# Performance work log

Measured on AMD Instinct MI355X. Metric: run time of the kernel, lower is better.

Reference implementation:

```python
import jax, jax.numpy as jnp
import numpy as np

N_P, N_A = 200_000, 100_000
D_P, D_A, H, OUT = 64, 64, 32, 1
E_PP, E_AP, E_PA = 3_200_000, 1_600_000, 1_600_000


def _lin(key, din, dout, bias=True):
    kw, kb = jax.random.split(key)
    W = jax.random.normal(kw, (din, dout), jnp.float32) * (1.0 / np.sqrt(din))
    if bias:
        b = jax.random.normal(kb, (dout,), jnp.float32) * 0.01
        return W, b
    return W


def setup_inputs() -> dict:
    key = jax.random.key(0)
    ks = jax.random.split(key, 24)
    inp = {}
    inp['x_paper'] = jax.random.normal(ks[0], (N_P, D_P), jnp.float32)
    inp['x_author'] = jax.random.normal(ks[1], (N_A, D_A), jnp.float32)
    inp['src_pp'] = jax.random.randint(ks[2], (E_PP,), 0, N_P)
    inp['dst_pp'] = jax.random.randint(ks[3], (E_PP,), 0, N_P)
    inp['src_ap'] = jax.random.randint(ks[4], (E_AP,), 0, N_A)
    inp['dst_ap'] = jax.random.randint(ks[5], (E_AP,), 0, N_P)
    inp['src_pa'] = jax.random.randint(ks[6], (E_PA,), 0, N_P)
    inp['dst_pa'] = jax.random.randint(ks[7], (E_PA,), 0, N_A)
    # Layer-1 SAGEConv weights per relation: lin_l (neighbor, with bias), lin_r (root, no bias)
    inp['Wl1_pp'], inp['bl1_pp'] = _lin(ks[8], D_P, H)
    inp['Wr1_pp'] = _lin(ks[9], D_P, H, bias=False)
    inp['Wl1_ap'], inp['bl1_ap'] = _lin(ks[10], D_A, H)
    inp['Wr1_ap'] = _lin(ks[11], D_P, H, bias=False)
    inp['Wl1_pa'], inp['bl1_pa'] = _lin(ks[12], D_P, H)
    inp['Wr1_pa'] = _lin(ks[13], D_A, H, bias=False)
    # Layer-2 SAGEConv weights (only relations feeding 'paper' affect the output)
    inp['Wl2_pp'], inp['bl2_pp'] = _lin(ks[14], H, H)
    inp['Wr2_pp'] = _lin(ks[15], H, H, bias=False)
    inp['Wl2_ap'], inp['bl2_ap'] = _lin(ks[16], H, H)
    inp['Wr2_ap'] = _lin(ks[17], H, H, bias=False)
    # Final classifier Linear(32, 1)
    inp['W_lin'], inp['b_lin'] = _lin(ks[18], H, OUT)
    return inp


def _sage_rel(x_src, x_dst, src, dst, Wl, bl, Wr):
    # SAGEConv: lin_l(mean_{j in N(i)} x_j) + lin_r(x_i)
    n_dst = x_dst.shape[0]
    agg = jax.ops.segment_sum(x_src[src], dst, num_segments=n_dst)
    cnt = jax.ops.segment_sum(jnp.ones((src.shape[0],), x_src.dtype), dst, num_segments=n_dst)
    mean = agg / jnp.maximum(cnt, 1.0)[:, None]
    return mean @ Wl + bl + x_dst @ Wr


def reference(x_paper, x_author, src_pp, dst_pp, src_ap, dst_ap, src_pa, dst_pa,
              Wl1_pp, bl1_pp, Wr1_pp, Wl1_ap, bl1_ap, Wr1_ap, Wl1_pa, bl1_pa, Wr1_pa,
              Wl2_pp, bl2_pp, Wr2_pp, Wl2_ap, bl2_ap, Wr2_ap, W_lin, b_lin):
    # Layer 1 (to_hetero: sum per-relation conv outputs per destination type), then relu
    p1 = (_sage_rel(x_paper, x_paper, src_pp, dst_pp, Wl1_pp, bl1_pp, Wr1_pp)
          + _sage_rel(x_author, x_paper, src_ap, dst_ap, Wl1_ap, bl1_ap, Wr1_ap))
    a1 = _sage_rel(x_paper, x_author, src_pa, dst_pa, Wl1_pa, bl1_pa, Wr1_pa)
    p1, a1 = jax.nn.relu(p1), jax.nn.relu(a1)
    # Layer 2: only 'paper' output is consumed downstream
    p2 = (_sage_rel(p1, p1, src_pp, dst_pp, Wl2_pp, bl2_pp, Wr2_pp)
          + _sage_rel(a1, p1, src_ap, dst_ap, Wl2_ap, bl2_ap, Wr2_ap))
    # model_config is None -> plain Linear, no sigmoid/softmax
    return p2 @ W_lin + b_lin
```

## Files before the change

kernel.cpp:

```cpp
#include <hip/hip_runtime.h>


typedef unsigned short ushort_t;
typedef __attribute__((ext_vector_type(8))) short bf16x8;
typedef __attribute__((ext_vector_type(4))) float f32x4;

#define PWBITS 9
#define PWIN   (1 << PWBITS)
#define PCHUNK 4096
#define CAPPAD 2048
#define FW_R   12

__device__ inline ushort_t f2bf(float f) {
    unsigned u = __float_as_uint(f);
    unsigned r = (u + 0x7FFFu + ((u >> 16) & 1u)) >> 16;
    return (ushort_t)r;
}
__device__ inline float bf2f_lo(unsigned u) { return __uint_as_float(u << 16); }
__device__ inline float bf2f_hi(unsigned u) { return __uint_as_float(u & 0xFFFF0000u); }
__device__ inline int ntl(const int* p) { return __builtin_nontemporal_load(p); }

__global__ void prep_weights(
    const float* __restrict__ Wl1_pp, const float* __restrict__ Wr1_pp,
    const float* __restrict__ Wl1_ap, const float* __restrict__ Wr1_ap,
    const float* __restrict__ Wl1_pa, const float* __restrict__ Wr1_pa,
    const float* __restrict__ bl1_pp, const float* __restrict__ bl1_ap,
    const float* __restrict__ bl1_pa,
    const float* __restrict__ Wl2_pp, const float* __restrict__ bl2_pp,
    const float* __restrict__ Wr2_pp,
    const float* __restrict__ Wl2_ap, const float* __restrict__ bl2_ap,
    const float* __restrict__ Wr2_ap,
    const float* __restrict__ W_lin, const float* __restrict__ b_lin,
    float* __restrict__ Wcomb_p,
    float* __restrict__ Wcomb_a,
    ushort_t* __restrict__ Wfrag_p,
    ushort_t* __restrict__ Wfrag_a,
    float* __restrict__ bias_p,
    float* __restrict__ bias_a,
    float* __restrict__ vv)
{
    int t = threadIdx.x;
    for (int idx = t; idx < 64 * 96; idx += 256) {
        int i = idx / 96, j = idx % 96;
        float v;
        if (j < 32)       v = Wl1_pp[i * 32 + j];
        else if (j < 64)  v = Wl1_pa[i * 32 + (j - 32)];
        else              v = Wr1_pp[i * 32 + (j - 64)] + Wr1_ap[i * 32 + (j - 64)];
        Wcomb_p[idx] = v;
    }
    for (int idx = t; idx < 64 * 64; idx += 256) {
        int i = idx / 64, j = idx % 64;
        Wcomb_a[idx] = (j < 32) ? Wl1_ap[i * 32 + j] : Wr1_pa[i * 32 + (j - 32)];
    }
    if (t < 32) {
        bias_p[t] = bl1_pp[t] + bl1_ap[t];
        bias_a[t] = bl1_pa[t];
        float vpp = 0.f, vr = 0.f, vap = 0.f;
        for (int j = 0; j < 32; ++j) {
            float wl = W_lin[j];
            vpp += Wl2_pp[t * 32 + j] * wl;
            vr  += (Wr2_pp[t * 32 + j] + Wr2_ap[t * 32 + j]) * wl;
            vap += Wl2_ap[t * 32 + j] * wl;
        }
        vv[t] = vpp; vv[32 + t] = vr; vv[96 + t] = vap;
    }
    if (t == 0) {
        float c = b_lin[0];
        for (int j = 0; j < 32; ++j) c += (bl2_pp[j] + bl2_ap[j]) * W_lin[j];
        vv[64] = c;
    }
    __syncthreads();
    for (int idx = t; idx < 12 * 64 * 8; idx += 256) {
        int f = idx >> 9, l = (idx >> 3) & 63, j = idx & 7;
        int nt = f >> 1, kh = f & 1;
        int k = kh * 32 + 8 * (l >> 4) + j;
        int n = nt * 16 + (l & 15);
        Wfrag_p[idx] = f2bf(Wcomb_p[k * 96 + n]);
    }
    for (int idx = t; idx < 8 * 64 * 8; idx += 256) {
        int f = idx >> 9, l = (idx >> 3) & 63, j = idx & 7;
        int nt = f >> 1, kh = f & 1;
        int k = kh * 32 + 8 * (l >> 4) + j;
        int n = nt * 16 + (l & 15);
        Wfrag_a[idx] = f2bf(Wcomb_a[k * 64 + n]);
    }
}

__global__ __launch_bounds__(256)
void partition3(
    const int* __restrict__ src0, const int* __restrict__ dst0, int E0,
    unsigned* __restrict__ bk0, int cap0, int nw0, int* __restrict__ wc0,
    const int* __restrict__ src1, const int* __restrict__ dst1, int E1,
    unsigned* __restrict__ bk1, int cap1, int nw1, int* __restrict__ wc1,
    const int* __restrict__ src2, const int* __restrict__ dst2, int E2,
    unsigned* __restrict__ bk2, int cap2, int nw2, int* __restrict__ wc2)
{
    __shared__ int lcnt[PWIN];
    __shared__ int lbase[PWIN];
    int nb0 = (E0 + PCHUNK - 1) / PCHUNK;
    int nb1 = (E1 + PCHUNK - 1) / PCHUNK;
    int b = blockIdx.x;
    const int* src; const int* dst; int E; unsigned* bk; int cap; int nw; int* wc; int chunk;
    if (b < nb0)            { src = src0; dst = dst0; E = E0; bk = bk0; cap = cap0; nw = nw0; wc = wc0; chunk = b; }
    else if (b < nb0 + nb1) { src = src1; dst = dst1; E = E1; bk = bk1; cap = cap1; nw = nw1; wc = wc1; chunk = b - nb0; }
    else                    { src = src2; dst = dst2; E = E2; bk = bk2; cap = cap2; nw = nw2; wc = wc2; chunk = b - nb0 - nb1; }
    int e0 = chunk * PCHUNK;
    int d_[16], s_[16];
#pragma unroll
    for (int r = 0; r < 4; ++r) {
        int base = e0 + r * 1024 + threadIdx.x * 4;
        if (base + 3 < E) {
            int4 dv = *(const int4*)(dst + base);
            int4 sv = *(const int4*)(src + base);
            d_[r * 4 + 0] = dv.x; d_[r * 4 + 1] = dv.y; d_[r * 4 + 2] = dv.z; d_[r * 4 + 3] = dv.w;
            s_[r * 4 + 0] = sv.x; s_[r * 4 + 1] = sv.y; s_[r * 4 + 2] = sv.z; s_[r * 4 + 3] = sv.w;
        } else {
#pragma unroll
            for (int k = 0; k < 4; ++k) {
                int e = base + k;
                d_[r * 4 + k] = (e < E) ? dst[e] : -1;
                s_[r * 4 + k] = 0;
            }
        }
    }
    for (int i = threadIdx.x; i < nw; i += 256) lcnt[i] = 0;
    __syncthreads();
#pragma unroll
    for (int k = 0; k < 16; ++k)
        if (d_[k] >= 0) atomicAdd(&lcnt[((unsigned)d_[k]) >> PWBITS], 1);
    __syncthreads();
    for (int i = threadIdx.x; i < nw; i += 256) {
        int c = lcnt[i];
        lbase[i] = (c > 0) ? atomicAdd(&wc[i * 16], c) : 0;
        lcnt[i] = 0;
    }
    __syncthreads();
#pragma unroll
    for (int k = 0; k < 16; ++k) {
        int d = d_[k];
        if (d >= 0) {
            int w = ((unsigned)d) >> PWBITS;
            int off = lbase[w] + atomicAdd(&lcnt[w], 1);
            if (off < cap)
                bk[(size_t)w * cap + off] =
                    (((unsigned)(d & (PWIN - 1))) << 18) | (unsigned)s_[k];
        }
    }
}

__global__ __launch_bounds__(256)
void fill_win3(
    const unsigned* __restrict__ bk0, const int* __restrict__ wc0, int cap0,
    int* __restrict__ csr0, int* __restrict__ cnt0, int* __restrict__ rs0, int N0, int nw0,
    const unsigned* __restrict__ bk1, const int* __restrict__ wc1, int cap1,
    int* __restrict__ csr1, int* __restrict__ cnt1, int* __restrict__ rs1, int N1, int nw1,
    const unsigned* __restrict__ bk2, const int* __restrict__ wc2, int cap2,
    int* __restrict__ csr2, int* __restrict__ cnt2, int* __restrict__ rs2, int N2, int nw2)
{
    __shared__ int lc[PWIN];
    __shared__ int wsum[4], wpre[4];
    int b = blockIdx.x;
    const unsigned* bk; const int* wc; int cap; int* csr; int* cnt; int* rs; int N; int w;
    if (b < nw0)            { bk = bk0; wc = wc0; cap = cap0; csr = csr0; cnt = cnt0; rs = rs0; N = N0; w = b; }
    else if (b < nw0 + nw1) { bk = bk1; wc = wc1; cap = cap1; csr = csr1; cnt = cnt1; rs = rs1; N = N1; w = b - nw0; }
    else                    { bk = bk2; wc = wc2; cap = cap2; csr = csr2; cnt = cnt2; rs = rs2; N = N2; w = b - nw0 - nw1; }
    int d0 = w << PWBITS;
    int sz = wc[w * 16]; if (sz > cap) sz = cap;
    const unsigned* bkt = bk + (size_t)w * cap;
    uint4 u[FW_R];
#pragma unroll
    for (int r = 0; r < FW_R; ++r) {
        int i4 = r * 1024 + threadIdx.x * 4;
        if (i4 + 3 < sz) {
            u[r] = *(const uint4*)(bkt + i4);
        } else {
            u[r].x = (i4 + 0 < sz) ? bkt[i4 + 0] : 0xFFFFFFFFu;
            u[r].y = (i4 + 1 < sz) ? bkt[i4 + 1] : 0xFFFFFFFFu;
            u[r].z = (i4 + 2 < sz) ? bkt[i4 + 2] : 0xFFFFFFFFu;
            u[r].w = (i4 + 3 < sz) ? bkt[i4 + 3] : 0xFFFFFFFFu;
        }
    }
    for (int i = threadIdx.x; i < PWIN; i += 256) lc[i] = 0;
    __syncthreads();
#pragma unroll
    for (int r = 0; r < FW_R; ++r) {
        if (u[r].x != 0xFFFFFFFFu) atomicAdd(&lc[u[r].x >> 18], 1);
        if (u[r].y != 0xFFFFFFFFu) atomicAdd(&lc[u[r].y >> 18], 1);
        if (u[r].z != 0xFFFFFFFFu) atomicAdd(&lc[u[r].z >> 18], 1);
        if (u[r].w != 0xFFFFFFFFu) atomicAdd(&lc[u[r].w >> 18], 1);
    }
    __syncthreads();
    {
        int i = threadIdx.x * 2;
        int d = d0 + i;
        if (d < N)     cnt[d] = lc[i];
        if (d + 1 < N) cnt[d + 1] = lc[i + 1];
    }
    int t2 = threadIdx.x * 2;
    int v0 = lc[t2], v1 = lc[t2 + 1];
    int ts = v0 + v1;
    int lane = threadIdx.x & 63;
    int wid = threadIdx.x >> 6;
    int incl = ts;
#pragma unroll
    for (int off = 1; off < 64; off <<= 1) {
        int o = __shfl_up(incl, off);
        if (lane >= off) incl += o;
    }
    if (lane == 63) wsum[wid] = incl;
    __syncthreads();
    if (threadIdx.x == 0) {
        int r = 0;
        for (int i = 0; i < 4; ++i) { wpre[i] = r; r += wsum[i]; }
    }
    __syncthreads();
    int run = w * cap + wpre[wid] + (incl - ts);
    lc[t2] = run;
    if (d0 + t2 < N) rs[d0 + t2] = run;
    run += v0;
    lc[t2 + 1] = run;
    if (d0 + t2 + 1 < N) rs[d0 + t2 + 1] = run;
    __syncthreads();
#pragma unroll
    for (int r = 0; r < FW_R; ++r) {
        if (u[r].x != 0xFFFFFFFFu) { int p = atomicAdd(&lc[u[r].x >> 18], 1); csr[p] = (int)(u[r].x & 0x3FFFFu); }
        if (u[r].y != 0xFFFFFFFFu) { int p = atomicAdd(&lc[u[r].y >> 18], 1); csr[p] = (int)(u[r].y & 0x3FFFFu); }
        if (u[r].z != 0xFFFFFFFFu) { int p = atomicAdd(&lc[u[r].z >> 18], 1); csr[p] = (int)(u[r].z & 0x3FFFFu); }
        if (u[r].w != 0xFFFFFFFFu) { int p = atomicAdd(&lc[u[r].w >> 18], 1); csr[p] = (int)(u[r].w & 0x3FFFFu); }
    }
}

__device__ inline bf16x8 cvt8(const float* p) {
    float4 a = *(const float4*)p;
    float4 b = *(const float4*)(p + 4);
    bf16x8 r;
    r[0] = (short)f2bf(a.x); r[1] = (short)f2bf(a.y);
    r[2] = (short)f2bf(a.z); r[3] = (short)f2bf(a.w);
    r[4] = (short)f2bf(b.x); r[5] = (short)f2bf(b.y);
    r[6] = (short)f2bf(b.z); r[7] = (short)f2bf(b.w);
    return r;
}

__global__ __launch_bounds__(256)
void proj_paper_mfma(const float* __restrict__ x, const ushort_t* __restrict__ Wfrag,
                     const float* __restrict__ bias,
                     ushort_t* __restrict__ h_pp, ushort_t* __restrict__ h_pa,
                     float* __restrict__ root_p, int N)
{
    int wave = threadIdx.x >> 6, lane = threadIdx.x & 63;
    int mbase = blockIdx.x * 64 + wave * 16;
    int row = lane & 15, grp = lane >> 4;
    int nA = mbase + row; if (nA > N - 1) nA = N - 1;
    const float* xr = x + (size_t)nA * 64 + grp * 8;
    bf16x8 a0 = cvt8(xr);
    bf16x8 a1 = cvt8(xr + 32);
    f32x4 acc0 = {0.f, 0.f, 0.f, 0.f}, acc1 = acc0, acc2 = acc0, acc3 = acc0;
    float bp0 = bias[row];
    float bp1 = bias[16 + row];
    f32x4 acc4 = {bp0, bp0, bp0, bp0};
    f32x4 acc5 = {bp1, bp1, bp1, bp1};
    const bf16x8* wf = (const bf16x8*)(Wfrag) + lane;
    acc0 = __builtin_amdgcn_mfma_f32_16x16x32_bf16(a0, wf[0 * 64], acc0, 0, 0, 0);
    acc0 = __builtin_amdgcn_mfma_f32_16x16x32_bf16(a1, wf[1 * 64], acc0, 0, 0, 0);
    acc1 = __builtin_amdgcn_mfma_f32_16x16x32_bf16(a0, wf[2 * 64], acc1, 0, 0, 0);
    acc1 = __builtin_amdgcn_mfma_f32_16x16x32_bf16(a1, wf[3 * 64], acc1, 0, 0, 0);
    acc2 = __builtin_amdgcn_mfma_f32_16x16x32_bf16(a0, wf[4 * 64], acc2, 0, 0, 0);
    acc2 = __builtin_amdgcn_mfma_f32_16x16x32_bf16(a1, wf[5 * 64], acc2, 0, 0, 0);
    acc3 = __builtin_amdgcn_mfma_f32_16x16x32_bf16(a0, wf[6 * 64], acc3, 0, 0, 0);
    acc3 = __builtin_amdgcn_mfma_f32_16x16x32_bf16(a1, wf[7 * 64], acc3, 0, 0, 0);
    acc4 = __builtin_amdgcn_mfma_f32_16x16x32_bf16(a0, wf[8 * 64], acc4, 0, 0, 0);
    acc4 = __builtin_amdgcn_mfma_f32_16x16x32_bf16(a1, wf[9 * 64], acc4, 0, 0, 0);
    acc5 = __builtin_amdgcn_mfma_f32_16x16x32_bf16(a0, wf[10 * 64], acc5, 0, 0, 0);
    acc5 = __builtin_amdgcn_mfma_f32_16x16x32_bf16(a1, wf[11 * 64], acc5, 0, 0, 0);
    int col = row;
    int node0 = mbase + grp * 4;
#pragma unroll
    for (int reg = 0; reg < 4; ++reg) {
        int nd = node0 + reg;
        if (nd < N) {
            size_t b32 = (size_t)nd * 32;
            h_pp[b32 + col]        = f2bf(acc0[reg]);
            h_pp[b32 + 16 + col]   = f2bf(acc1[reg]);
            h_pa[b32 + col]        = f2bf(acc2[reg]);
            h_pa[b32 + 16 + col]   = f2bf(acc3[reg]);
            root_p[b32 + col]      = acc4[reg];
            root_p[b32 + 16 + col] = acc5[reg];
        }
    }
}

__global__ __launch_bounds__(256)
void proj_author_mfma(const float* __restrict__ x, const ushort_t* __restrict__ Wfrag,
                      const float* __restrict__ bias,
                      ushort_t* __restrict__ h_ap, float* __restrict__ root_a, int N)
{
    int wave = threadIdx.x >> 6, lane = threadIdx.x & 63;
    int mbase = blockIdx.x * 64 + wave * 16;
    int row = lane & 15, grp = lane >> 4;
    int nA = mbase + row; if (nA > N - 1) nA = N - 1;
    const float* xr = x + (size_t)nA * 64 + grp * 8;
    bf16x8 a0 = cvt8(xr);
    bf16x8 a1 = cvt8(xr + 32);
    f32x4 acc0 = {0.f, 0.f, 0.f, 0.f}, acc1 = acc0;
    float bp0 = bias[row];
    float bp1 = bias[16 + row];
    f32x4 acc2 = {bp0, bp0, bp0, bp0};
    f32x4 acc3 = {bp1, bp1, bp1, bp1};
    const bf16x8* wf = (const bf16x8*)(Wfrag) + lane;
    acc0 = __builtin_amdgcn_mfma_f32_16x16x32_bf16(a0, wf[0 * 64], acc0, 0, 0, 0);
    acc0 = __builtin_amdgcn_mfma_f32_16x16x32_bf16(a1, wf[1 * 64], acc0, 0, 0, 0);
    acc1 = __builtin_amdgcn_mfma_f32_16x16x32_bf16(a0, wf[2 * 64], acc1, 0, 0, 0);
    acc1 = __builtin_amdgcn_mfma_f32_16x16x32_bf16(a1, wf[3 * 64], acc1, 0, 0, 0);
    acc2 = __builtin_amdgcn_mfma_f32_16x16x32_bf16(a0, wf[4 * 64], acc2, 0, 0, 0);
    acc2 = __builtin_amdgcn_mfma_f32_16x16x32_bf16(a1, wf[5 * 64], acc2, 0, 0, 0);
    acc3 = __builtin_amdgcn_mfma_f32_16x16x32_bf16(a0, wf[6 * 64], acc3, 0, 0, 0);
    acc3 = __builtin_amdgcn_mfma_f32_16x16x32_bf16(a1, wf[7 * 64], acc3, 0, 0, 0);
    int col = row;
    int node0 = mbase + grp * 4;
#pragma unroll
    for (int reg = 0; reg < 4; ++reg) {
        int nd = node0 + reg;
        if (nd < N) {
            size_t b32 = (size_t)nd * 32;
            h_ap[b32 + col]        = f2bf(acc0[reg]);
            h_ap[b32 + 16 + col]   = f2bf(acc1[reg]);
            root_a[b32 + col]      = acc2[reg];
            root_a[b32 + 16 + col] = acc3[reg];
        }
    }
}

#define ACC8(A, U) \
    A[0] += bf2f_lo((U).x); A[1] += bf2f_hi((U).x); \
    A[2] += bf2f_lo((U).y); A[3] += bf2f_hi((U).y); \
    A[4] += bf2f_lo((U).z); A[5] += bf2f_hi((U).z); \
    A[6] += bf2f_lo((U).w); A[7] += bf2f_hi((U).w);

__global__ __launch_bounds__(256, 8)
void pull_paper(const ushort_t* __restrict__ h_pp, const ushort_t* __restrict__ h_ap,
                const float* __restrict__ root,
                const int* __restrict__ csr_pp, const int* __restrict__ rs_pp,
                const int* __restrict__ cnt_pp,
                const int* __restrict__ csr_ap, const int* __restrict__ rs_ap,
                const int* __restrict__ cnt_ap,
                const float* __restrict__ vv,
                float* __restrict__ s_pp, float* __restrict__ out, int N)
{
    __shared__ float v0[32], v1[32];
    __shared__ float c2s;
    if (threadIdx.x < 32) { v0[threadIdx.x] = vv[threadIdx.x]; v1[threadIdx.x] = vv[32 + threadIdx.x]; }
    if (threadIdx.x == 0) c2s = vv[64];
    __syncthreads();
    int n = blockIdx.x * 64 + (threadIdx.x >> 2);
    if (n >= N) return;
    int c = threadIdx.x & 3;
    float a[8];
#pragma unroll
    for (int k = 0; k < 8; ++k) a[k] = 0.f;
    int s1 = rs_pp[n], k1 = cnt_pp[n], e1 = s1 + k1;
    int j = s1;
    for (; j + 4 <= e1; j += 4) {
        int i0 = ntl(csr_pp + j), i1 = ntl(csr_pp + j + 1);
        int i2 = ntl(csr_pp + j + 2), i3 = ntl(csr_pp + j + 3);
        uint4 u0 = ((const uint4*)(h_pp + (size_t)i0 * 32))[c];
        uint4 u1 = ((const uint4*)(h_pp + (size_t)i1 * 32))[c];
        uint4 u2 = ((const uint4*)(h_pp + (size_t)i2 * 32))[c];
        uint4 u3 = ((const uint4*)(h_pp + (size_t)i3 * 32))[c];
        ACC8(a, u0) ACC8(a, u1) ACC8(a, u2) ACC8(a, u3)
    }
    for (; j < e1; ++j) {
        uint4 u0 = ((const uint4*)(h_pp + (size_t)ntl(csr_pp + j) * 32))[c];
        ACC8(a, u0)
    }
    float b[8];
#pragma unroll
    for (int k = 0; k < 8; ++k) b[k] = 0.f;
    int s2 = rs_ap[n], k2 = cnt_ap[n], e2 = s2 + k2;
    j = s2;
    for (; j + 4 <= e2; j += 4) {
        int i0 = ntl(csr_ap + j), i1 = ntl(csr_ap + j + 1);
        int i2 = ntl(csr_ap + j + 2), i3 = ntl(csr_ap + j + 3);
        uint4 u0 = ((const uint4*)(h_ap + (size_t)i0 * 32))[c];
        uint4 u1 = ((const uint4*)(h_ap + (size_t)i1 * 32))[c];
        uint4 u2 = ((const uint4*)(h_ap + (size_t)i2 * 32))[c];
        uint4 u3 = ((const uint4*)(h_ap + (size_t)i3 * 32))[c];
        ACC8(b, u0) ACC8(b, u1) ACC8(b, u2) ACC8(b, u3)
    }
    for (; j < e2; ++j) {
        uint4 u0 = ((const uint4*)(h_ap + (size_t)ntl(csr_ap + j) * 32))[c];
        ACC8(b, u0)
    }
    float ipp = 1.0f / fmaxf((float)k1, 1.0f);
    float iap = 1.0f / fmaxf((float)k2, 1.0f);
    const float* rt = root + (size_t)n * 32 + 8 * c;
    float d0 = 0.f, d1 = 0.f;
#pragma unroll
    for (int k = 0; k < 8; ++k) {
        float p = fmaxf(rt[k] + a[k] * ipp + b[k] * iap, 0.f);
        d0 += p * v0[8 * c + k];
        d1 += p * v1[8 * c + k];
    }
    d0 += __shfl_xor(d0, 1); d0 += __shfl_xor(d0, 2);
    d1 += __shfl_xor(d1, 1); d1 += __shfl_xor(d1, 2);
    if (c == 0) { s_pp[n] = d0; out[n] = d1 + c2s; }
}

__global__ __launch_bounds__(256, 8)
void pull_author(const ushort_t* __restrict__ h_pa, const float* __restrict__ root,
                 const int* __restrict__ csr_pa, const int* __restrict__ rs_pa,
                 const int* __restrict__ cnt_pa,
                 const float* __restrict__ vv, float* __restrict__ s_ap, int N)
{
    __shared__ float v0[32];
    if (threadIdx.x < 32) v0[threadIdx.x] = vv[96 + threadIdx.x];
    __syncthreads();
    int n = blockIdx.x * 64 + (threadIdx.x >> 2);
    if (n >= N) return;
    int c = threadIdx.x & 3;
    float a[8];
#pragma unroll
    for (int k = 0; k < 8; ++k) a[k] = 0.f;
    int s1 = rs_pa[n], k1 = cnt_pa[n], e1 = s1 + k1;
    int j = s1;
    for (; j + 4 <= e1; j += 4) {
        int i0 = ntl(csr_pa + j), i1 = ntl(csr_pa + j + 1);
        int i2 = ntl(csr_pa + j + 2), i3 = ntl(csr_pa + j + 3);
        uint4 u0 = ((const uint4*)(h_pa + (size_t)i0 * 32))[c];
        uint4 u1 = ((const uint4*)(h_pa + (size_t)i1 * 32))[c];
        uint4 u2 = ((const uint4*)(h_pa + (size_t)i2 * 32))[c];
        uint4 u3 = ((const uint4*)(h_pa + (size_t)i3 * 32))[c];
        ACC8(a, u0) ACC8(a, u1) ACC8(a, u2) ACC8(a, u3)
    }
    for (; j < e1; ++j) {
        uint4 u0 = ((const uint4*)(h_pa + (size_t)ntl(csr_pa + j) * 32))[c];
        ACC8(a, u0)
    }
    float ip = 1.0f / fmaxf((float)k1, 1.0f);
    const float* rt = root + (size_t)n * 32 + 8 * c;
    float d0 = 0.f;
#pragma unroll
    for (int k = 0; k < 8; ++k) {
        float p = fmaxf(rt[k] + a[k] * ip, 0.f);
        d0 += p * v0[8 * c + k];
    }
    d0 += __shfl_xor(d0, 1); d0 += __shfl_xor(d0, 2);
    if (c == 0) s_ap[n] = d0;
}

__global__ __launch_bounds__(256, 8)
void pull2(const float* __restrict__ s_pp, const float* __restrict__ s_ap,
           const int* __restrict__ csr_pp, const int* __restrict__ rs_pp,
           const int* __restrict__ cnt_pp,
           const int* __restrict__ csr_ap, const int* __restrict__ rs_ap,
           const int* __restrict__ cnt_ap,
           float* __restrict__ out, int N)
{
    int g = (blockIdx.x * blockDim.x + threadIdx.x) >> 2;
    int c = threadIdx.x & 3;
    if (g >= N) return;
    int s1 = rs_pp[g], k1 = cnt_pp[g], e1 = s1 + k1;
    float t = 0.f;
    for (int j = s1 + c; j < e1; j += 4) t += s_pp[ntl(csr_pp + j)];
    int s2 = rs_ap[g], k2 = cnt_ap[g], e2 = s2 + k2;
    float u = 0.f;
    for (int j = s2 + c; j < e2; j += 4) u += s_ap[ntl(csr_ap + j)];
    t += __shfl_xor(t, 1); t += __shfl_xor(t, 2);
    u += __shfl_xor(u, 1); u += __shfl_xor(u, 2);
    if (c == 0) {
        out[g] += t / fmaxf((float)k1, 1.f) + u / fmaxf((float)k2, 1.f);
    }
}

extern "C" void kernel_launch(void* const* d_in, const int* in_sizes, int n_in,
                              void* d_out, int out_size, void* d_ws, size_t ws_size,
                              hipStream_t stream)
{
    const float* x_paper  = (const float*)d_in[0];
    const float* x_author = (const float*)d_in[1];
    const int* src_pp = (const int*)d_in[2];
    const int* dst_pp = (const int*)d_in[3];
    const int* src_ap = (const int*)d_in[4];
    const int* dst_ap = (const int*)d_in[5];
    const int* src_pa = (const int*)d_in[6];
    const int* dst_pa = (const int*)d_in[7];
    const float* Wl1_pp = (const float*)d_in[8];
    const float* bl1_pp = (const float*)d_in[9];
    const float* Wr1_pp = (const float*)d_in[10];
    const float* Wl1_ap = (const float*)d_in[11];
    const float* bl1_ap = (const float*)d_in[12];
    const float* Wr1_ap = (const float*)d_in[13];
    const float* Wl1_pa = (const float*)d_in[14];
    const float* bl1_pa = (const float*)d_in[15];
    const float* Wr1_pa = (const float*)d_in[16];
    const float* Wl2_pp = (const float*)d_in[17];
    const float* bl2_pp = (const float*)d_in[18];
    const float* Wr2_pp = (const float*)d_in[19];
    const float* Wl2_ap = (const float*)d_in[20];
    const float* bl2_ap = (const float*)d_in[21];
    const float* Wr2_ap = (const float*)d_in[22];
    const float* W_lin  = (const float*)d_in[23];
    const float* b_lin  = (const float*)d_in[24];

    const int NP = in_sizes[0] / 64;
    const int NA = in_sizes[1] / 64;
    const int E_PP = in_sizes[2];
    const int E_AP = in_sizes[4];
    const int E_PA = in_sizes[6];

    const int nw_pp = (NP + PWIN - 1) >> PWBITS;
    const int nw_ap = nw_pp;
    const int nw_pa = (NA + PWIN - 1) >> PWBITS;
    const int cap_pp = ((E_PP / nw_pp + CAPPAD) + 3) & ~3;
    const int cap_ap = ((E_AP / nw_ap + CAPPAD) + 3) & ~3;
    const int cap_pa = ((E_PA / nw_pa + CAPPAD) + 3) & ~3;

    char* wp = (char*)d_ws;
    int* wcur = (int*)wp;             wp += (size_t)3 * PWIN * 16 * 4;
    unsigned* bk_pp = (unsigned*)wp;  wp += (size_t)nw_pp * cap_pp * 4;
    unsigned* bk_ap = (unsigned*)wp;  wp += (size_t)nw_ap * cap_ap * 4;
    unsigned* bk_pa = (unsigned*)wp;  wp += (size_t)nw_pa * cap_pa * 4;
    int* csr_pp = (int*)wp;           wp += (size_t)nw_pp * cap_pp * 4;
    int* csr_ap = (int*)wp;           wp += (size_t)nw_ap * cap_ap * 4;
    int* csr_pa = (int*)wp;           wp += (size_t)nw_pa * cap_pa * 4;
    int* cnt    = (int*)wp;           wp += (size_t)(2 * NP + NA) * 4;
    int* rs     = (int*)wp;           wp += (size_t)(2 * NP + NA) * 4;
    ushort_t* h_pp = (ushort_t*)wp;   wp += (size_t)NP * 32 * 2;
    ushort_t* h_pa = (ushort_t*)wp;   wp += (size_t)NP * 32 * 2;
    ushort_t* h_ap = (ushort_t*)wp;   wp += (size_t)NA * 32 * 2;
    float* root_a = (float*)wp;       wp += (size_t)NA * 32 * 4;
    float* s_pp   = (float*)wp;       wp += (size_t)NP * 4;
    float* s_ap   = (float*)wp;       wp += (size_t)NA * 4;
    float* Wcomb_p = (float*)wp;      wp += 64 * 96 * 4;
    float* Wcomb_a = (float*)wp;      wp += 64 * 64 * 4;
    ushort_t* Wfrag_p = (ushort_t*)wp; wp += 12 * 64 * 8 * 2;
    ushort_t* Wfrag_a = (ushort_t*)wp; wp += 8 * 64 * 8 * 2;
    float* bias_p = (float*)wp;       wp += 32 * 4;
    float* bias_a = (float*)wp;       wp += 32 * 4;
    float* vv     = (float*)wp;       wp += 128 * 4;
    float* root_p = (float*)bk_pp;

    int* cnt_pp = cnt,  * cnt_ap = cnt + NP,  * cnt_pa = cnt + 2 * NP;
    int* rs_pp  = rs,   * rs_ap  = rs + NP,   * rs_pa  = rs + 2 * NP;

    float* out = (float*)d_out;

    hipMemsetAsync(wcur, 0, (size_t)3 * PWIN * 16 * 4, stream);

    prep_weights<<<1, 256, 0, stream>>>(
        Wl1_pp, Wr1_pp, Wl1_ap, Wr1_ap, Wl1_pa, Wr1_pa,
        bl1_pp, bl1_ap, bl1_pa,
        Wl2_pp, bl2_pp, Wr2_pp, Wl2_ap, bl2_ap, Wr2_ap,
        W_lin, b_lin, Wcomb_p, Wcomb_a, Wfrag_p, Wfrag_a, bias_p, bias_a, vv);

    int nb_total = (E_PP + PCHUNK - 1) / PCHUNK + (E_AP + PCHUNK - 1) / PCHUNK
                 + (E_PA + PCHUNK - 1) / PCHUNK;
    partition3<<<nb_total, 256, 0, stream>>>(
        src_pp, dst_pp, E_PP, bk_pp, cap_pp, nw_pp, wcur + 0,
        src_ap, dst_ap, E_AP, bk_ap, cap_ap, nw_ap, wcur + PWIN * 16,
        src_pa, dst_pa, E_PA, bk_pa, cap_pa, nw_pa, wcur + 2 * PWIN * 16);

    fill_win3<<<nw_pp + nw_ap + nw_pa, 256, 0, stream>>>(
        bk_pp, wcur + 0,            cap_pp, csr_pp, cnt_pp, rs_pp, NP, nw_pp,
        bk_ap, wcur + PWIN * 16,    cap_ap, csr_ap, cnt_ap, rs_ap, NP, nw_ap,
        bk_pa, wcur + 2 * PWIN * 16, cap_pa, csr_pa, cnt_pa, rs_pa, NA, nw_pa);

    proj_paper_mfma<<<(NP + 63) / 64, 256, 0, stream>>>(
        x_paper, Wfrag_p, bias_p, h_pp, h_pa, root_p, NP);
    proj_author_mfma<<<(NA + 63) / 64, 256, 0, stream>>>(
        x_author, Wfrag_a, bias_a, h_ap, root_a, NA);

    pull_paper<<<(NP + 63) / 64, 256, 0, stream>>>(
        h_pp, h_ap, root_p, csr_pp, rs_pp, cnt_pp, csr_ap, rs_ap, cnt_ap,
        vv, s_pp, out, NP);
    pull_author<<<(NA + 63) / 64, 256, 0, stream>>>(
        h_pa, root_a, csr_pa, rs_pa, cnt_pa, vv, s_ap, NA);

    pull2<<<((size_t)NP * 4 + 255) / 256, 256, 0, stream>>>(
        s_pp, s_ap, csr_pp, rs_pp, cnt_pp, csr_ap, rs_ap, cnt_ap, out, NP);
}
```

Before: 375.6 us.

## Merge paper/author projection and pull kernels into single launches with interleaved gathers

```diff
diff --git a/kernel.cpp b/kernel.cpp
--- a/kernel.cpp
+++ b/kernel.cpp
@@ -242,90 +242,85 @@
 }
 
 __global__ __launch_bounds__(256)
-void proj_paper_mfma(const float* __restrict__ x, const ushort_t* __restrict__ Wfrag,
-                     const float* __restrict__ bias,
-                     ushort_t* __restrict__ h_pp, ushort_t* __restrict__ h_pa,
-                     float* __restrict__ root_p, int N)
+void proj_all(const float* __restrict__ xp, const float* __restrict__ xa,
+              const ushort_t* __restrict__ Wfp, const ushort_t* __restrict__ Wfa,
+              const float* __restrict__ bias_p, const float* __restrict__ bias_a,
+              ushort_t* __restrict__ h_pp, ushort_t* __restrict__ h_pa,
+              ushort_t* __restrict__ h_ap,
+              float* __restrict__ root_p, float* __restrict__ root_a,
+              int NP, int NA, int pbp)
 {
     int wave = threadIdx.x >> 6, lane = threadIdx.x & 63;
-    int mbase = blockIdx.x * 64 + wave * 16;
     int row = lane & 15, grp = lane >> 4;
-    int nA = mbase + row; if (nA > N - 1) nA = N - 1;
-    const float* xr = x + (size_t)nA * 64 + grp * 8;
-    bf16x8 a0 = cvt8(xr);
-    bf16x8 a1 = cvt8(xr + 32);
-    f32x4 acc0 = {0.f, 0.f, 0.f, 0.f}, acc1 = acc0, acc2 = acc0, acc3 = acc0;
-    float bp0 = bias[row];
-    float bp1 = bias[16 + row];
-    f32x4 acc4 = {bp0, bp0, bp0, bp0};
-    f32x4 acc5 = {bp1, bp1, bp1, bp1};
-    const bf16x8* wf = (const bf16x8*)(Wfrag) + lane;
-    acc0 = __builtin_amdgcn_mfma_f32_16x16x32_bf16(a0, wf[0 * 64], acc0, 0, 0, 0);
-    acc0 = __builtin_amdgcn_mfma_f32_16x16x32_bf16(a1, wf[1 * 64], acc0, 0, 0, 0);
-    acc1 = __builtin_amdgcn_mfma_f32_16x16x32_bf16(a0, wf[2 * 64], acc1, 0, 0, 0);
-    acc1 = __builtin_amdgcn_mfma_f32_16x16x32_bf16(a1, wf[3 * 64], acc1, 0, 0, 0);
-    acc2 = __builtin_amdgcn_mfma_f32_16x16x32_bf16(a0, wf[4 * 64], acc2, 0, 0, 0);
-    acc2 = __builtin_amdgcn_mfma_f32_16x16x32_bf16(a1, wf[5 * 64], acc2, 0, 0, 0);
-    acc3 = __builtin_amdgcn_mfma_f32_16x16x32_bf16(a0, wf[6 * 64], acc3, 0, 0, 0);
-    acc3 = __builtin_amdgcn_mfma_f32_16x16x32_bf16(a1, wf[7 * 64], acc3, 0, 0, 0);
-    acc4 = __builtin_amdgcn_mfma_f32_16x16x32_bf16(a0, wf[8 * 64], acc4, 0, 0, 0);
-    acc4 = __builtin_amdgcn_mfma_f32_16x16x32_bf16(a1, wf[9 * 64], acc4, 0, 0, 0);
-    acc5 = __builtin_amdgcn_mfma_f32_16x16x32_bf16(a0, wf[10 * 64], acc5, 0, 0, 0);
-    acc5 = __builtin_amdgcn_mfma_f32_16x16x32_bf16(a1, wf[11 * 64], acc5, 0, 0, 0);
-    int col = row;
-    int node0 = mbase + grp * 4;
-#pragma unroll
-    for (int reg = 0; reg < 4; ++reg) {
-        int nd = node0 + reg;
-        if (nd < N) {
-            size_t b32 = (size_t)nd * 32;
-            h_pp[b32 + col]        = f2bf(acc0[reg]);
-            h_pp[b32 + 16 + col]   = f2bf(acc1[reg]);
-            h_pa[b32 + col]        = f2bf(acc2[reg]);
-            h_pa[b32 + 16 + col]   = f2bf(acc3[reg]);
-            root_p[b32 + col]      = acc4[reg];
-            root_p[b32 + 16 + col] = acc5[reg];
-        }
-    }
-}
-
-__global__ __launch_bounds__(256)
-void proj_author_mfma(const float* __restrict__ x, const ushort_t* __restrict__ Wfrag,
-                      const float* __restrict__ bias,
-                      ushort_t* __restrict__ h_ap, float* __restrict__ root_a, int N)
-{
-    int wave = threadIdx.x >> 6, lane = threadIdx.x & 63;
-    int mbase = blockIdx.x * 64 + wave * 16;
-    int row = lane & 15, grp = lane >> 4;
-    int nA = mbase + row; if (nA > N - 1) nA = N - 1;
-    const float* xr = x + (size_t)nA * 64 + grp * 8;
-    bf16x8 a0 = cvt8(xr);
-    bf16x8 a1 = cvt8(xr + 32);
-    f32x4 acc0 = {0.f, 0.f, 0.f, 0.f}, acc1 = acc0;
-    float bp0 = bias[row];
-    float bp1 = bias[16 + row];
-    f32x4 acc2 = {bp0, bp0, bp0, bp0};
-    f32x4 acc3 = {bp1, bp1, bp1, bp1};
-    const bf16x8* wf = (const bf16x8*)(Wfrag) + lane;
-    acc0 = __builtin_amdgcn_mfma_f32_16x16x32_bf16(a0, wf[0 * 64], acc0, 0, 0, 0);
-    acc0 = __builtin_amdgcn_mfma_f32_16x16x32_bf16(a1, wf[1 * 64], acc0, 0, 0, 0);
-    acc1 = __builtin_amdgcn_mfma_f32_16x16x32_bf16(a0, wf[2 * 64], acc1, 0, 0, 0);
-    acc1 = __builtin_amdgcn_mfma_f32_16x16x32_bf16(a1, wf[3 * 64], acc1, 0, 0, 0);
-    acc2 = __builtin_amdgcn_mfma_f32_16x16x32_bf16(a0, wf[4 * 64], acc2, 0, 0, 0);
-    acc2 = __builtin_amdgcn_mfma_f32_16x16x32_bf16(a1, wf[5 * 64], acc2, 0, 0, 0);
-    acc3 = __builtin_amdgcn_mfma_f32_16x16x32_bf16(a0, wf[6 * 64], acc3, 0, 0, 0);
-    acc3 = __builtin_amdgcn_mfma_f32_16x16x32_bf16(a1, wf[7 * 64], acc3, 0, 0, 0);
-    int col = row;
-    int node0 = mbase + grp * 4;
-#pragma unroll
-    for (int reg = 0; reg < 4; ++reg) {
-        int nd = node0 + reg;
-        if (nd < N) {
-            size_t b32 = (size_t)nd * 32;
-            h_ap[b32 + col]        = f2bf(acc0[reg]);
-            h_ap[b32 + 16 + col]   = f2bf(acc1[reg]);
-            root_a[b32 + col]      = acc2[reg];
-            root_a[b32 + 16 + col] = acc3[reg];
+    if (blockIdx.x < pbp) {
+        int mbase = blockIdx.x * 64 + wave * 16;
+        int nA = mbase + row; if (nA > NP - 1) nA = NP - 1;
+        const float* xr = xp + (size_t)nA * 64 + grp * 8;
+        bf16x8 a0 = cvt8(xr);
+        bf16x8 a1 = cvt8(xr + 32);
+        f32x4 acc0 = {0.f, 0.f, 0.f, 0.f}, acc1 = acc0, acc2 = acc0, acc3 = acc0;
+        float bp0 = bias_p[row];
+        float bp1 = bias_p[16 + row];
+        f32x4 acc4 = {bp0, bp0, bp0, bp0};
+        f32x4 acc5 = {bp1, bp1, bp1, bp1};
+        const bf16x8* wf = (const bf16x8*)(Wfp) + lane;
+        acc0 = __builtin_amdgcn_mfma_f32_16x16x32_bf16(a0, wf[0 * 64], acc0, 0, 0, 0);
+        acc0 = __builtin_amdgcn_mfma_f32_16x16x32_bf16(a1, wf[1 * 64], acc0, 0, 0, 0);
+        acc1 = __builtin_amdgcn_mfma_f32_16x16x32_bf16(a0, wf[2 * 64], acc1, 0, 0, 0);
+        acc1 = __builtin_amdgcn_mfma_f32_16x16x32_bf16(a1, wf[3 * 64], acc1, 0, 0, 0);
+        acc2 = __builtin_amdgcn_mfma_f32_16x16x32_bf16(a0, wf[4 * 64], acc2, 0, 0, 0);
+        acc2 = __builtin_amdgcn_mfma_f32_16x16x32_bf16(a1, wf[5 * 64], acc2, 0, 0, 0);
+        acc3 = __builtin_amdgcn_mfma_f32_16x16x32_bf16(a0, wf[6 * 64], acc3, 0, 0, 0);
+        acc3 = __builtin_amdgcn_mfma_f32_16x16x32_bf16(a1, wf[7 * 64], acc3, 0, 0, 0);
+        acc4 = __builtin_amdgcn_mfma_f32_16x16x32_bf16(a0, wf[8 * 64], acc4, 0, 0, 0);
+        acc4 = __builtin_amdgcn_mfma_f32_16x16x32_bf16(a1, wf[9 * 64], acc4, 0, 0, 0);
+        acc5 = __builtin_amdgcn_mfma_f32_16x16x32_bf16(a0, wf[10 * 64], acc5, 0, 0, 0);
+        acc5 = __builtin_amdgcn_mfma_f32_16x16x32_bf16(a1, wf[11 * 64], acc5, 0, 0, 0);
+        int node0 = mbase + grp * 4;
+#pragma unroll
+        for (int reg = 0; reg < 4; ++reg) {
+            int nd = node0 + reg;
+            if (nd < NP) {
+                size_t b32 = (size_t)nd * 32;
+                h_pp[b32 + row]        = f2bf(acc0[reg]);
+                h_pp[b32 + 16 + row]   = f2bf(acc1[reg]);
+                h_pa[b32 + row]        = f2bf(acc2[reg]);
+                h_pa[b32 + 16 + row]   = f2bf(acc3[reg]);
+                root_p[b32 + row]      = acc4[reg];
+                root_p[b32 + 16 + row] = acc5[reg];
+            }
+        }
+    } else {
+        int mbase = (blockIdx.x - pbp) * 64 + wave * 16;
+        int nA = mbase + row; if (nA > NA - 1) nA = NA - 1;
+        const float* xr = xa + (size_t)nA * 64 + grp * 8;
+        bf16x8 a0 = cvt8(xr);
+        bf16x8 a1 = cvt8(xr + 32);
+        f32x4 acc0 = {0.f, 0.f, 0.f, 0.f}, acc1 = acc0;
+        float bp0 = bias_a[row];
+        float bp1 = bias_a[16 + row];
+        f32x4 acc2 = {bp0, bp0, bp0, bp0};
+        f32x4 acc3 = {bp1, bp1, bp1, bp1};
+        const bf16x8* wf = (const bf16x8*)(Wfa) + lane;
+        acc0 = __builtin_amdgcn_mfma_f32_16x16x32_bf16(a0, wf[0 * 64], acc0, 0, 0, 0);
+        acc0 = __builtin_amdgcn_mfma_f32_16x16x32_bf16(a1, wf[1 * 64], acc0, 0, 0, 0);
+        acc1 = __builtin_amdgcn_mfma_f32_16x16x32_bf16(a0, wf[2 * 64], acc1, 0, 0, 0);
+        acc1 = __builtin_amdgcn_mfma_f32_16x16x32_bf16(a1, wf[3 * 64], acc1, 0, 0, 0);
+        acc2 = __builtin_amdgcn_mfma_f32_16x16x32_bf16(a0, wf[4 * 64], acc2, 0, 0, 0);
+        acc2 = __builtin_amdgcn_mfma_f32_16x16x32_bf16(a1, wf[5 * 64], acc2, 0, 0, 0);
+        acc3 = __builtin_amdgcn_mfma_f32_16x16x32_bf16(a0, wf[6 * 64], acc3, 0, 0, 0);
+        acc3 = __builtin_amdgcn_mfma_f32_16x16x32_bf16(a1, wf[7 * 64], acc3, 0, 0, 0);
+        int node0 = mbase + grp * 4;
+#pragma unroll
+        for (int reg = 0; reg < 4; ++reg) {
+            int nd = node0 + reg;
+            if (nd < NA) {
+                size_t b32 = (size_t)nd * 32;
+                h_ap[b32 + row]        = f2bf(acc0[reg]);
+                h_ap[b32 + 16 + row]   = f2bf(acc1[reg]);
+                root_a[b32 + row]      = acc2[reg];
+                root_a[b32 + 16 + row] = acc3[reg];
+            }
         }
     }
 }
@@ -336,115 +331,125 @@
     A[4] += bf2f_lo((U).z); A[5] += bf2f_hi((U).z); \
     A[6] += bf2f_lo((U).w); A[7] += bf2f_hi((U).w);
 
-__global__ __launch_bounds__(256, 8)
-void pull_paper(const ushort_t* __restrict__ h_pp, const ushort_t* __restrict__ h_ap,
-                const float* __restrict__ root,
-                const int* __restrict__ csr_pp, const int* __restrict__ rs_pp,
-                const int* __restrict__ cnt_pp,
-                const int* __restrict__ csr_ap, const int* __restrict__ rs_ap,
-                const int* __restrict__ cnt_ap,
-                const float* __restrict__ vv,
-                float* __restrict__ s_pp, float* __restrict__ out, int N)
+__global__ __launch_bounds__(256, 6)
+void pull_all(const ushort_t* __restrict__ h_pp, const ushort_t* __restrict__ h_ap,
+              const ushort_t* __restrict__ h_pa,
+              const float* __restrict__ root_p, const float* __restrict__ root_a,
+              const int* __restrict__ csr_pp, const int* __restrict__ rs_pp,
+              const int* __restrict__ cnt_pp,
+              const int* __restrict__ csr_ap, const int* __restrict__ rs_ap,
+              const int* __restrict__ cnt_ap,
+              const int* __restrict__ csr_pa, const int* __restrict__ rs_pa,
+              const int* __restrict__ cnt_pa,
+              const float* __restrict__ vv,
+              float* __restrict__ s_pp, float* __restrict__ s_ap,
+              float* __restrict__ out, int NP, int NA, int pbp)
 {
     __shared__ float v0[32], v1[32];
     __shared__ float c2s;
-    if (threadIdx.x < 32) { v0[threadIdx.x] = vv[threadIdx.x]; v1[threadIdx.x] = vv[32 + threadIdx.x]; }
-    if (threadIdx.x == 0) c2s = vv[64];
-    __syncthreads();
-    int n = blockIdx.x * 64 + (threadIdx.x >> 2);
-    if (n >= N) return;
     int c = threadIdx.x & 3;
-    float a[8];
-#pragma unroll
-    for (int k = 0; k < 8; ++k) a[k] = 0.f;
-    int s1 = rs_pp[n], k1 = cnt_pp[n], e1 = s1 + k1;
-    int j = s1;
-    for (; j + 4 <= e1; j += 4) {
-        int i0 = ntl(csr_pp + j), i1 = ntl(csr_pp + j + 1);
-        int i2 = ntl(csr_pp + j + 2), i3 = ntl(csr_pp + j + 3);
-        uint4 u0 = ((const uint4*)(h_pp + (size_t)i0 * 32))[c];
-        uint4 u1 = ((const uint4*)(h_pp + (size_t)i1 * 32))[c];
-        uint4 u2 = ((const uint4*)(h_pp + (size_t)i2 * 32))[c];
-        uint4 u3 = ((const uint4*)(h_pp + (size_t)i3 * 32))[c];
-        ACC8(a, u0) ACC8(a, u1) ACC8(a, u2) ACC8(a, u3)
-    }
-    for (; j < e1; ++j) {
-        uint4 u0 = ((const uint4*)(h_pp + (size_t)ntl(csr_pp + j) * 32))[c];
-        ACC8(a, u0)
-    }
-    float b[8];
-#pragma unroll
-    for (int k = 0; k < 8; ++k) b[k] = 0.f;
-    int s2 = rs_ap[n], k2 = cnt_ap[n], e2 = s2 + k2;
-    j = s2;
-    for (; j + 4 <= e2; j += 4) {
-        int i0 = ntl(csr_ap + j), i1 = ntl(csr_ap + j + 1);
-        int i2 = ntl(csr_ap + j + 2), i3 = ntl(csr_ap + j + 3);
-        uint4 u0 = ((const uint4*)(h_ap + (size_t)i0 * 32))[c];
-        uint4 u1 = ((const uint4*)(h_ap + (size_t)i1 * 32))[c];
-        uint4 u2 = ((const uint4*)(h_ap + (size_t)i2 * 32))[c];
-        uint4 u3 = ((const uint4*)(h_ap + (size_t)i3 * 32))[c];
-        ACC8(b, u0) ACC8(b, u1) ACC8(b, u2) ACC8(b, u3)
-    }
-    for (; j < e2; ++j) {
-        uint4 u0 = ((const uint4*)(h_ap + (size_t)ntl(csr_ap + j) * 32))[c];
-        ACC8(b, u0)
-    }
-    float ipp = 1.0f / fmaxf((float)k1, 1.0f);
-    float iap = 1.0f / fmaxf((float)k2, 1.0f);
-    const float* rt = root + (size_t)n * 32 + 8 * c;
-    float d0 = 0.f, d1 = 0.f;
-#pragma unroll
-    for (int k = 0; k < 8; ++k) {
-        float p = fmaxf(rt[k] + a[k] * ipp + b[k] * iap, 0.f);
-        d0 += p * v0[8 * c + k];
-        d1 += p * v1[8 * c + k];
-    }
-    d0 += __shfl_xor(d0, 1); d0 += __shfl_xor(d0, 2);
-    d1 += __shfl_xor(d1, 1); d1 += __shfl_xor(d1, 2);
-    if (c == 0) { s_pp[n] = d0; out[n] = d1 + c2s; }
-}
-
-__global__ __launch_bounds__(256, 8)
-void pull_author(const ushort_t* __restrict__ h_pa, const float* __restrict__ root,
-                 const int* __restrict__ csr_pa, const int* __restrict__ rs_pa,
-                 const int* __restrict__ cnt_pa,
-                 const float* __restrict__ vv, float* __restrict__ s_ap, int N)
-{
-    __shared__ float v0[32];
-    if (threadIdx.x < 32) v0[threadIdx.x] = vv[96 + threadIdx.x];
-    __syncthreads();
-    int n = blockIdx.x * 64 + (threadIdx.x >> 2);
-    if (n >= N) return;
-    int c = threadIdx.x & 3;
-    float a[8];
-#pragma unroll
-    for (int k = 0; k < 8; ++k) a[k] = 0.f;
-    int s1 = rs_pa[n], k1 = cnt_pa[n], e1 = s1 + k1;
-    int j = s1;
-    for (; j + 4 <= e1; j += 4) {
-        int i0 = ntl(csr_pa + j), i1 = ntl(csr_pa + j + 1);
-        int i2 = ntl(csr_pa + j + 2), i3 = ntl(csr_pa + j + 3);
-        uint4 u0 = ((const uint4*)(h_pa + (size_t)i0 * 32))[c];
-        uint4 u1 = ((const uint4*)(h_pa + (size_t)i1 * 32))[c];
-        uint4 u2 = ((const uint4*)(h_pa + (size_t)i2 * 32))[c];
-        uint4 u3 = ((const uint4*)(h_pa + (size_t)i3 * 32))[c];
-        ACC8(a, u0) ACC8(a, u1) ACC8(a, u2) ACC8(a, u3)
-    }
-    for (; j < e1; ++j) {
-        uint4 u0 = ((const uint4*)(h_pa + (size_t)ntl(csr_pa + j) * 32))[c];
-        ACC8(a, u0)
-    }
-    float ip = 1.0f / fmaxf((float)k1, 1.0f);
-    const float* rt = root + (size_t)n * 32 + 8 * c;
-    float d0 = 0.f;
-#pragma unroll
-    for (int k = 0; k < 8; ++k) {
-        float p = fmaxf(rt[k] + a[k] * ip, 0.f);
-        d0 += p * v0[8 * c + k];
-    }
-    d0 += __shfl_xor(d0, 1); d0 += __shfl_xor(d0, 2);
-    if (c == 0) s_ap[n] = d0;
+    if (blockIdx.x < pbp) {
+        if (threadIdx.x < 32) { v0[threadIdx.x] = vv[threadIdx.x]; v1[threadIdx.x] = vv[32 + threadIdx.x]; }
+        if (threadIdx.x == 0) c2s = vv[64];
+        __syncthreads();
+        int n = blockIdx.x * 64 + (threadIdx.x >> 2);
+        if (n >= NP) return;
+        float a[8], b[8];
+#pragma unroll
+        for (int k = 0; k < 8; ++k) { a[k] = 0.f; b[k] = 0.f; }
+        int s1 = rs_pp[n], k1 = cnt_pp[n], e1 = s1 + k1;
+        int s2 = rs_ap[n], k2 = cnt_ap[n], e2 = s2 + k2;
+        int j1 = s1, j2 = s2;
+        while (j1 + 4 <= e1 && j2 + 4 <= e2) {
+            int i0 = ntl(csr_pp + j1), i1 = ntl(csr_pp + j1 + 1);
+            int i2 = ntl(csr_pp + j1 + 2), i3 = ntl(csr_pp + j1 + 3);
+            int g0 = ntl(csr_ap + j2), g1 = ntl(csr_ap + j2 + 1);
+            int g2 = ntl(csr_ap + j2 + 2), g3 = ntl(csr_ap + j2 + 3);
+            uint4 u0 = ((const uint4*)(h_pp + (size_t)i0 * 32))[c];
+            uint4 u1 = ((const uint4*)(h_pp + (size_t)i1 * 32))[c];
+            uint4 u2 = ((const uint4*)(h_pp + (size_t)i2 * 32))[c];
+            uint4 u3 = ((const uint4*)(h_pp + (size_t)i3 * 32))[c];
+            uint4 w0 = ((const uint4*)(h_ap + (size_t)g0 * 32))[c];
+            uint4 w1 = ((const uint4*)(h_ap + (size_t)g1 * 32))[c];
+            uint4 w2 = ((const uint4*)(h_ap + (size_t)g2 * 32))[c];
+            uint4 w3 = ((const uint4*)(h_ap + (size_t)g3 * 32))[c];
+            ACC8(a, u0) ACC8(a, u1) ACC8(a, u2) ACC8(a, u3)
+            ACC8(b, w0) ACC8(b, w1) ACC8(b, w2) ACC8(b, w3)
+            j1 += 4; j2 += 4;
+        }
+        for (; j1 + 4 <= e1; j1 += 4) {
+            int i0 = ntl(csr_pp + j1), i1 = ntl(csr_pp + j1 + 1);
+            int i2 = ntl(csr_pp + j1 + 2), i3 = ntl(csr_pp + j1 + 3);
+            uint4 u0 = ((const uint4*)(h_pp + (size_t)i0 * 32))[c];
+            uint4 u1 = ((const uint4*)(h_pp + (size_t)i1 * 32))[c];
+            uint4 u2 = ((const uint4*)(h_pp + (size_t)i2 * 32))[c];
+            uint4 u3 = ((const uint4*)(h_pp + (size_t)i3 * 32))[c];
+            ACC8(a, u0) ACC8(a, u1) ACC8(a, u2) ACC8(a, u3)
+        }
+        for (; j1 < e1; ++j1) {
+            uint4 u0 = ((const uint4*)(h_pp + (size_t)ntl(csr_pp + j1) * 32))[c];
+            ACC8(a, u0)
+        }
+        for (; j2 + 4 <= e2; j2 += 4) {
+            int g0 = ntl(csr_ap + j2), g1 = ntl(csr_ap + j2 + 1);
+            int g2 = ntl(csr_ap + j2 + 2), g3 = ntl(csr_ap + j2 + 3);
+            uint4 w0 = ((const uint4*)(h_ap + (size_t)g0 * 32))[c];
+            uint4 w1 = ((const uint4*)(h_ap + (size_t)g1 * 32))[c];
+            uint4 w2 = ((const uint4*)(h_ap + (size_t)g2 * 32))[c];
+            uint4 w3 = ((const uint4*)(h_ap + (size_t)g3 * 32))[c];
+            ACC8(b, w0) ACC8(b, w1) ACC8(b, w2) ACC8(b, w3)
+        }
+        for (; j2 < e2; ++j2) {
+            uint4 w0 = ((const uint4*)(h_ap + (size_t)ntl(csr_ap + j2) * 32))[c];
+            ACC8(b, w0)
+        }
+        float ipp = 1.0f / fmaxf((float)k1, 1.0f);
+        float iap = 1.0f / fmaxf((float)k2, 1.0f);
+        const float* rt = root_p + (size_t)n * 32 + 8 * c;
+        float d0 = 0.f, d1 = 0.f;
+#pragma unroll
+        for (int k = 0; k < 8; ++k) {
+            float p = fmaxf(rt[k] + a[k] * ipp + b[k] * iap, 0.f);
+            d0 += p * v0[8 * c + k];
+            d1 += p * v1[8 * c + k];
+        }
+        d0 += __shfl_xor(d0, 1); d0 += __shfl_xor(d0, 2);
+        d1 += __shfl_xor(d1, 1); d1 += __shfl_xor(d1, 2);
+        if (c == 0) { s_pp[n] = d0; out[n] = d1 + c2s; }
+    } else {
+        if (threadIdx.x < 32) v0[threadIdx.x] = vv[96 + threadIdx.x];
+        __syncthreads();
+        int n = (blockIdx.x - pbp) * 64 + (threadIdx.x >> 2);
+        if (n >= NA) return;
+        float a[8];
+#pragma unroll
+        for (int k = 0; k < 8; ++k) a[k] = 0.f;
+        int s1 = rs_pa[n], k1 = cnt_pa[n], e1 = s1 + k1;
+        int j = s1;
+        for (; j + 4 <= e1; j += 4) {
+            int i0 = ntl(csr_pa + j), i1 = ntl(csr_pa + j + 1);
+            int i2 = ntl(csr_pa + j + 2), i3 = ntl(csr_pa + j + 3);
+            uint4 u0 = ((const uint4*)(h_pa + (size_t)i0 * 32))[c];
+            uint4 u1 = ((const uint4*)(h_pa + (size_t)i1 * 32))[c];
+            uint4 u2 = ((const uint4*)(h_pa + (size_t)i2 * 32))[c];
+            uint4 u3 = ((const uint4*)(h_pa + (size_t)i3 * 32))[c];
+            ACC8(a, u0) ACC8(a, u1) ACC8(a, u2) ACC8(a, u3)
+        }
+        for (; j < e1; ++j) {
+            uint4 u0 = ((const uint4*)(h_pa + (size_t)ntl(csr_pa + j) * 32))[c];
+            ACC8(a, u0)
+        }
+        float ip = 1.0f / fmaxf((float)k1, 1.0f);
+        const float* rt = root_a + (size_t)n * 32 + 8 * c;
+        float d0 = 0.f;
+#pragma unroll
+        for (int k = 0; k < 8; ++k) {
+            float p = fmaxf(rt[k] + a[k] * ip, 0.f);
+            d0 += p * v0[8 * c + k];
+        }
+        d0 += __shfl_xor(d0, 1); d0 += __shfl_xor(d0, 2);
+        if (c == 0) s_ap[n] = d0;
+    }
 }
 
 __global__ __launch_bounds__(256, 8)
@@ -564,16 +569,16 @@
         bk_ap, wcur + PWIN * 16,    cap_ap, csr_ap, cnt_ap, rs_ap, NP, nw_ap,
         bk_pa, wcur + 2 * PWIN * 16, cap_pa, csr_pa, cnt_pa, rs_pa, NA, nw_pa);
 
-    proj_paper_mfma<<<(NP + 63) / 64, 256, 0, stream>>>(
-        x_paper, Wfrag_p, bias_p, h_pp, h_pa, root_p, NP);
-    proj_author_mfma<<<(NA + 63) / 64, 256, 0, stream>>>(
-        x_author, Wfrag_a, bias_a, h_ap, root_a, NA);
-
-    pull_paper<<<(NP + 63) / 64, 256, 0, stream>>>(
-        h_pp, h_ap, root_p, csr_pp, rs_pp, cnt_pp, csr_ap, rs_ap, cnt_ap,
-        vv, s_pp, out, NP);
-    pull_author<<<(NA + 63) / 64, 256, 0, stream>>>(
-        h_pa, root_a, csr_pa, rs_pa, cnt_pa, vv, s_ap, NA);
+    int pbp_proj = (NP + 63) / 64;
+    int pba_proj = (NA + 63) / 64;
+    proj_all<<<pbp_proj + pba_proj, 256, 0, stream>>>(
+        x_paper, x_author, Wfrag_p, Wfrag_a, bias_p, bias_a,
+        h_pp, h_pa, h_ap, root_p, root_a, NP, NA, pbp_proj);
+
+    pull_all<<<pbp_proj + pba_proj, 256, 0, stream>>>(
+        h_pp, h_ap, h_pa, root_p, root_a,
+        csr_pp, rs_pp, cnt_pp, csr_ap, rs_ap, cnt_ap, csr_pa, rs_pa, cnt_pa,
+        vv, s_pp, s_ap, out, NP, NA, pbp_proj);
 
     pull2<<<((size_t)NP * 4 + 255) / 256, 256, 0, stream>>>(
         s_pp, s_ap, csr_pp, rs_pp, cnt_pp, csr_ap, rs_ap, cnt_ap, out, NP);
```

Result: no change. 378.3 us (+0.7%).
